# Performance work log

Measured on AMD Instinct MI355X. Metric: run time of the kernel, lower is better.

The kernel has to match this reference:

```python
import jax, jax.numpy as jnp
import numpy as np

B, N, H = 4, 1024, 64

def setup_inputs() -> dict:
    key = jax.random.key(0)
    k1, k2, k3 = jax.random.split(key, 3)
    x = jax.random.normal(k1, (B, N, H), dtype=jnp.float32)
    # nn.Linear(2H, H): weight [H, 2H], bias [H]
    s1 = 1.0 / np.sqrt(2 * H)
    W1 = jax.random.uniform(k2, (H, 2 * H), minval=-s1, maxval=s1, dtype=jnp.float32)
    b1 = jnp.zeros((H,), dtype=jnp.float32)
    # nn.Linear(H, 1): weight [1, H], bias [1]
    s2 = 1.0 / np.sqrt(H)
    W2 = jax.random.uniform(k3, (1, H), minval=-s2, maxval=s2, dtype=jnp.float32)
    b2 = jnp.zeros((1,), dtype=jnp.float32)
    return {"x": x, "W1": W1, "b1": b1, "W2": W2, "b2": b2}

def reference(x, W1, b1, W2, b2):
    # cat([x_i, x_j]) @ W1.T == x_i @ W1a.T + x_j @ W1b.T  (decomposed; same math)
    W1a, W1b = W1[:, :x.shape[-1]], W1[:, x.shape[-1]:]
    hi = jnp.einsum('bid,hd->bih', x, W1a)            # [B,N,H]
    hj = jnp.einsum('bjd,hd->bjh', x, W1b)            # [B,N,H]
    h = jax.nn.relu(hi[:, :, None, :] + hj[:, None, :, :] + b1)  # [B,N,N,H]
    logits = jnp.einsum('bijh,h->bij', h, W2[0]) + b2[0]          # [B,N,N]
    attn = jax.nn.softmax(logits, axis=-1)
    updated = jnp.einsum('bij,bjd->bid', attn, x)     # [B,N,H]
    return updated, attn
```

## Files before the change

kernel.cpp:

```cpp
#include <hip/hip_runtime.h>

#define ATTN_OFF 262144

#define WS_HIT   0
#define WS_HJT   262144
#define WS_LOG   524288
#define WS_SMAX  4718592
#define WS_SSUM  4784128
#define WS_ROWM  4849664
#define WS_ROWI  4853760
#define WS_PART  4857856

typedef float4 f4;
__device__ __forceinline__ f4 ld4(const float* p) { return *reinterpret_cast<const f4*>(p); }
__device__ __forceinline__ void st4(float* p, f4 v) { *reinterpret_cast<f4*>(p) = v; }

__global__ __launch_bounds__(256, 4)
void ka_proj(const float* __restrict__ x, const float* __restrict__ W1,
             const float* __restrict__ b1,
             float* __restrict__ hiT, float* __restrict__ hjT) {
    __shared__ float xT[64 * 68];
    __shared__ float w1T[64 * 68];
    const int t  = threadIdx.x;
    const int i0 = blockIdx.x * 64;
    const int b  = blockIdx.y;
    const int z  = blockIdx.z;
    const int lo = t & 15;
    const int dq = t >> 4;
#pragma unroll
    for (int p = 0; p < 4; ++p) {
        const int il = p * 16 + lo;
        f4 v = ld4(&x[(size_t)(b * 1024 + i0 + il) * 64 + dq * 4]);
        xT[(dq * 4 + 0) * 68 + il] = v.x;
        xT[(dq * 4 + 1) * 68 + il] = v.y;
        xT[(dq * 4 + 2) * 68 + il] = v.z;
        xT[(dq * 4 + 3) * 68 + il] = v.w;
        f4 w = ld4(&W1[(size_t)il * 128 + z * 64 + dq * 4]);
        w1T[(dq * 4 + 0) * 68 + il] = w.x;
        w1T[(dq * 4 + 1) * 68 + il] = w.y;
        w1T[(dq * 4 + 2) * 68 + il] = w.z;
        w1T[(dq * 4 + 3) * 68 + il] = w.w;
    }
    __syncthreads();
    const int tx = t & 15;
    const int ty = t >> 4;
    float acc[4][4];
    if (z == 0) {
        f4 bv = ld4(&b1[tx * 4]);
        float ba[4] = {bv.x, bv.y, bv.z, bv.w};
#pragma unroll
        for (int ii = 0; ii < 4; ++ii)
#pragma unroll
            for (int cc = 0; cc < 4; ++cc) acc[ii][cc] = ba[cc];
    } else {
#pragma unroll
        for (int ii = 0; ii < 4; ++ii)
#pragma unroll
            for (int cc = 0; cc < 4; ++cc) acc[ii][cc] = 0.f;
    }
#pragma unroll 8
    for (int d = 0; d < 64; ++d) {
        f4 xv = ld4(&xT[d * 68 + ty * 4]);
        f4 wv = ld4(&w1T[d * 68 + tx * 4]);
        float xa[4] = {xv.x, xv.y, xv.z, xv.w};
        float wa[4] = {wv.x, wv.y, wv.z, wv.w};
#pragma unroll
        for (int ii = 0; ii < 4; ++ii)
#pragma unroll
            for (int cc = 0; cc < 4; ++cc)
                acc[ii][cc] = fmaf(xa[ii], wa[cc], acc[ii][cc]);
    }
    float* outp = z ? hjT : hiT;
#pragma unroll
    for (int cc = 0; cc < 4; ++cc) {
        f4 o = make_float4(acc[0][cc], acc[1][cc], acc[2][cc], acc[3][cc]);
        st4(&outp[(size_t)(b * 64 + tx * 4 + cc) * 1024 + i0 + ty * 4], o);
    }
}

__global__ __launch_bounds__(256, 2)
void kb_logits(const float* __restrict__ hiT, const float* __restrict__ hjT,
               const float* __restrict__ W2, float* __restrict__ logits,
               float* __restrict__ smax, float* __restrict__ ssum) {
    __shared__ float s_hi[64 * 128];
    __shared__ float s_hj[64 * 64];
    __shared__ float s_w2[64];
    const int t  = threadIdx.x;
    const int jT = blockIdx.x;
    const int iT = blockIdx.y;
    const int b  = blockIdx.z;
#pragma unroll
    for (int p = 0; p < 8; ++p) {
        const int idx = p * 256 + t;
        const int h   = idx >> 5;
        const int c4  = (idx & 31) * 4;
        st4(&s_hi[h * 128 + c4], ld4(&hiT[(size_t)(b * 64 + h) * 1024 + iT * 128 + c4]));
    }
#pragma unroll
    for (int p = 0; p < 4; ++p) {
        const int idx = p * 256 + t;
        const int h   = idx >> 4;
        const int c4  = (idx & 15) * 4;
        st4(&s_hj[h * 64 + c4], ld4(&hjT[(size_t)(b * 64 + h) * 1024 + jT * 64 + c4]));
    }
    if (t < 16) st4(&s_w2[t * 4], ld4(&W2[t * 4]));
    __syncthreads();
    const int tx = t & 15;
    const int ty = t >> 4;
    float acc[8][4];
#pragma unroll
    for (int ii = 0; ii < 8; ++ii)
#pragma unroll
        for (int jj = 0; jj < 4; ++jj) acc[ii][jj] = 0.f;
#pragma unroll 2
    for (int h = 0; h < 64; ++h) {
        f4 a0 = ld4(&s_hi[h * 128 + ty * 8]);
        f4 a1 = ld4(&s_hi[h * 128 + ty * 8 + 4]);
        f4 bv = ld4(&s_hj[h * 64 + tx * 4]);
        const float w = s_w2[h];
        float aa[8] = {a0.x, a0.y, a0.z, a0.w, a1.x, a1.y, a1.z, a1.w};
        float bb[4] = {bv.x, bv.y, bv.z, bv.w};
#pragma unroll
        for (int ii = 0; ii < 8; ++ii)
#pragma unroll
            for (int jj = 0; jj < 4; ++jj)
                acc[ii][jj] = fmaf(fmaxf(aa[ii] + bb[jj], 0.f), w, acc[ii][jj]);
    }
#pragma unroll
    for (int ii = 0; ii < 8; ++ii) {
        const int row = b * 1024 + iT * 128 + ty * 8 + ii;
        f4 o = make_float4(acc[ii][0], acc[ii][1], acc[ii][2], acc[ii][3]);
        st4(&logits[(size_t)row * 1024 + jT * 64 + tx * 4], o);
        float m = fmaxf(fmaxf(acc[ii][0], acc[ii][1]), fmaxf(acc[ii][2], acc[ii][3]));
#pragma unroll
        for (int d = 1; d < 16; d <<= 1) m = fmaxf(m, __shfl_xor(m, d));
        float s = __expf(acc[ii][0] - m) + __expf(acc[ii][1] - m) +
                  __expf(acc[ii][2] - m) + __expf(acc[ii][3] - m);
#pragma unroll
        for (int d = 1; d < 16; d <<= 1) s += __shfl_xor(s, d);
        if (tx == 0) {
            smax[jT * 4096 + row] = m;
            ssum[jT * 4096 + row] = s;
        }
    }
}

__global__ __launch_bounds__(256)
void kredux(const float* __restrict__ smax, const float* __restrict__ ssum,
            float* __restrict__ rowM, float* __restrict__ rowInv) {
    const int r = blockIdx.x * 256 + threadIdx.x;
    float mv[16], sv[16];
#pragma unroll
    for (int c = 0; c < 16; ++c) { mv[c] = smax[c * 4096 + r]; sv[c] = ssum[c * 4096 + r]; }
    float M = mv[0];
#pragma unroll
    for (int c = 1; c < 16; ++c) M = fmaxf(M, mv[c]);
    float L = 0.f;
#pragma unroll
    for (int c = 0; c < 16; ++c) L += sv[c] * __expf(mv[c] - M);
    rowM[r]   = M;
    rowInv[r] = 1.0f / L;
}

__global__ __launch_bounds__(256)
void kd_av(const float* __restrict__ logits, const float* __restrict__ rowM,
           const float* __restrict__ rowInv, const float* __restrict__ x,
           float* __restrict__ attn, float* __restrict__ part) {
    __shared__ float s_p[64 * 260];
    __shared__ float s_x[64 * 64];
    __shared__ float s_m[256];
    __shared__ float s_il[256];
    const int t  = threadIdx.x;
    const int ks = blockIdx.x;
    const int iT = blockIdx.y;
    const int b  = blockIdx.z;
    const int i0 = iT * 256;
    const int j0 = ks * 64;
    const int gr = b * 1024 + i0;
    s_m[t]  = rowM[gr + t];
    s_il[t] = rowInv[gr + t];
#pragma unroll
    for (int p = 0; p < 4; ++p) {
        const int idx = p * 256 + t;
        const int j   = idx >> 4;
        const int d4  = (idx & 15) * 4;
        st4(&s_x[j * 64 + d4], ld4(&x[(size_t)(b * 1024 + j0 + j) * 64 + d4]));
    }
    __syncthreads();
#pragma unroll 4
    for (int it = 0; it < 16; ++it) {
        const int idx = it * 256 + t;
        const int rl  = idx >> 4;
        const int j4  = (idx & 15) * 4;
        f4 v = ld4(&logits[(size_t)(gr + rl) * 1024 + j0 + j4]);
        const float m  = s_m[rl];
        const float il = s_il[rl];
        f4 pv;
        pv.x = __expf(v.x - m) * il;
        pv.y = __expf(v.y - m) * il;
        pv.z = __expf(v.z - m) * il;
        pv.w = __expf(v.w - m) * il;
        st4(&attn[(size_t)(gr + rl) * 1024 + j0 + j4], pv);
        s_p[(j4 + 0) * 260 + rl] = pv.x;
        s_p[(j4 + 1) * 260 + rl] = pv.y;
        s_p[(j4 + 2) * 260 + rl] = pv.z;
        s_p[(j4 + 3) * 260 + rl] = pv.w;
    }
    __syncthreads();
    const int tx = t & 7;
    const int ty = t >> 3;
    float acc[8][8];
#pragma unroll
    for (int ii = 0; ii < 8; ++ii)
#pragma unroll
        for (int dd = 0; dd < 8; ++dd) acc[ii][dd] = 0.f;
#pragma unroll 2
    for (int j = 0; j < 64; ++j) {
        f4 a0 = ld4(&s_p[j * 260 + ty * 8]);
        f4 a1 = ld4(&s_p[j * 260 + ty * 8 + 4]);
        f4 b0 = ld4(&s_x[j * 64 + tx * 8]);
        f4 b1 = ld4(&s_x[j * 64 + tx * 8 + 4]);
        float aa[8] = {a0.x, a0.y, a0.z, a0.w, a1.x, a1.y, a1.z, a1.w};
        float bb[8] = {b0.x, b0.y, b0.z, b0.w, b1.x, b1.y, b1.z, b1.w};
#pragma unroll
        for (int ii = 0; ii < 8; ++ii)
#pragma unroll
            for (int dd = 0; dd < 8; ++dd)
                acc[ii][dd] = fmaf(aa[ii], bb[dd], acc[ii][dd]);
    }
#pragma unroll
    for (int ii = 0; ii < 8; ++ii) {
        const size_t o = (size_t)(ks * 4096 + gr + ty * 8 + ii) * 64 + tx * 8;
        st4(&part[o],     make_float4(acc[ii][0], acc[ii][1], acc[ii][2], acc[ii][3]));
        st4(&part[o + 4], make_float4(acc[ii][4], acc[ii][5], acc[ii][6], acc[ii][7]));
    }
}

__global__ __launch_bounds__(256)
void ke_reduce(const float* __restrict__ part, float* __restrict__ out) {
    const int g = blockIdx.x * 256 + threadIdx.x;
    f4 a = ld4(&part[(size_t)g * 4]);
#pragma unroll
    for (int ks = 1; ks < 16; ++ks) {
        f4 v = ld4(&part[(size_t)ks * 262144 + g * 4]);
        a.x += v.x; a.y += v.y; a.z += v.z; a.w += v.w;
    }
    st4(&out[(size_t)g * 4], a);
}

extern "C" void kernel_launch(void* const* d_in, const int* in_sizes, int n_in,
                              void* d_out, int out_size, void* d_ws, size_t ws_size,
                              hipStream_t stream) {
    const float* x  = (const float*)d_in[0];
    const float* W1 = (const float*)d_in[1];
    const float* b1 = (const float*)d_in[2];
    const float* W2 = (const float*)d_in[3];
    float* out = (float*)d_out;
    float* ws  = (float*)d_ws;
    float* hiT    = ws + WS_HIT;
    float* hjT    = ws + WS_HJT;
    float* logits = ws + WS_LOG;
    float* smax   = ws + WS_SMAX;
    float* ssum   = ws + WS_SSUM;
    float* rowM   = ws + WS_ROWM;
    float* rowInv = ws + WS_ROWI;
    float* part   = ws + WS_PART;

    ka_proj  <<<dim3(16, 4, 2),  256, 0, stream>>>(x, W1, b1, hiT, hjT);
    kb_logits<<<dim3(16, 8, 4),  256, 0, stream>>>(hiT, hjT, W2, logits, smax, ssum);
    kredux   <<<dim3(16),        256, 0, stream>>>(smax, ssum, rowM, rowInv);
    kd_av    <<<dim3(16, 4, 4),  256, 0, stream>>>(logits, rowM, rowInv, x,
                                                   out + ATTN_OFF, part);
    ke_reduce<<<dim3(256),       256, 0, stream>>>(part, out);
}
```

Measured before the change: 118.3 us.

## Switch pairwise logits and AV to packed fp16 dot2, fuse reductions with atomics

Stores the projections, logits and the probability/x tiles as packed fp16 and uses v_dot2 (fp16 pairs accumulated in fp32) for both the relu-weighted logit sum and the attn@x product. This halves the logits workspace traffic and shared-memory footprint. It folds the row max/sum reduction into kd_av and replaces the split-K partial buffer and its reduce kernel with atomicAdd into an output zeroed by ka_proj, cutting two launches. The cost is reduced precision in the logits and attention weights, and nondeterministic float atomics.

```diff
diff --git a/kernel.cpp b/kernel.cpp
--- a/kernel.cpp
+++ b/kernel.cpp
@@ -2,29 +2,44 @@
 
 #define ATTN_OFF 262144
 
-#define WS_HIT   0
-#define WS_HJT   262144
-#define WS_LOG   524288
-#define WS_SMAX  4718592
-#define WS_SSUM  4784128
-#define WS_ROWM  4849664
-#define WS_ROWI  4853760
-#define WS_PART  4857856
+#define WS_HIP  0
+#define WS_HJP  131072
+#define WS_L16  262144
+#define WS_SMAX 2359296
+#define WS_SSUM 2424832
 
 typedef float4 f4;
+typedef _Float16 h2v __attribute__((ext_vector_type(2)));
+
+union F4H { f4 f; h2v h[4]; };
+union F2H { float2 f; h2v h[2]; };
+
 __device__ __forceinline__ f4 ld4(const float* p) { return *reinterpret_cast<const f4*>(p); }
 __device__ __forceinline__ void st4(float* p, f4 v) { *reinterpret_cast<f4*>(p) = v; }
+__device__ __forceinline__ float fdot2f(h2v a, h2v b, float c) {
+    return __builtin_amdgcn_fdot2(a, b, c, false);
+}
+__device__ __forceinline__ h2v pack2(float a, float b) {
+    h2v r; r.x = (_Float16)a; r.y = (_Float16)b; return r;
+}
 
 __global__ __launch_bounds__(256, 4)
 void ka_proj(const float* __restrict__ x, const float* __restrict__ W1,
              const float* __restrict__ b1,
-             float* __restrict__ hiT, float* __restrict__ hjT) {
+             h2v* __restrict__ hiP, h2v* __restrict__ hjP, float* __restrict__ outz) {
     __shared__ float xT[64 * 68];
     __shared__ float w1T[64 * 68];
     const int t  = threadIdx.x;
     const int i0 = blockIdx.x * 64;
     const int b  = blockIdx.y;
     const int z  = blockIdx.z;
+    {
+        const int bid = blockIdx.x + blockIdx.y * 16 + blockIdx.z * 64;
+        const int zi  = (bid * 256 + t) * 2;
+        f4 zv = make_float4(0.f, 0.f, 0.f, 0.f);
+        st4(&outz[(size_t)zi * 4], zv);
+        st4(&outz[(size_t)(zi + 1) * 4], zv);
+    }
     const int lo = t & 15;
     const int dq = t >> 4;
 #pragma unroll
@@ -70,40 +85,49 @@
             for (int cc = 0; cc < 4; ++cc)
                 acc[ii][cc] = fmaf(xa[ii], wa[cc], acc[ii][cc]);
     }
-    float* outp = z ? hjT : hiT;
-#pragma unroll
-    for (int cc = 0; cc < 4; ++cc) {
-        f4 o = make_float4(acc[0][cc], acc[1][cc], acc[2][cc], acc[3][cc]);
-        st4(&outp[(size_t)(b * 64 + tx * 4 + cc) * 1024 + i0 + ty * 4], o);
-    }
-}
-
-__global__ __launch_bounds__(256, 2)
-void kb_logits(const float* __restrict__ hiT, const float* __restrict__ hjT,
-               const float* __restrict__ W2, float* __restrict__ logits,
+    h2v* outp = z ? hjP : hiP;
+#pragma unroll
+    for (int p = 0; p < 2; ++p) {
+        F4H u;
+#pragma unroll
+        for (int ii = 0; ii < 4; ++ii)
+            u.h[ii] = pack2(acc[ii][p * 2 + 0], acc[ii][p * 2 + 1]);
+        st4((float*)&outp[(size_t)(b * 32 + tx * 2 + p) * 1024 + i0 + ty * 4], u.f);
+    }
+}
+
+__global__ __launch_bounds__(256, 4)
+void kb_logits(const h2v* __restrict__ hiP, const h2v* __restrict__ hjP,
+               const float* __restrict__ W2, _Float16* __restrict__ l16,
                float* __restrict__ smax, float* __restrict__ ssum) {
-    __shared__ float s_hi[64 * 128];
-    __shared__ float s_hj[64 * 64];
-    __shared__ float s_w2[64];
+    __shared__ __align__(16) h2v s_hi[32 * 128];
+    __shared__ __align__(16) h2v s_hj[32 * 64];
+    __shared__ h2v s_w2[32];
     const int t  = threadIdx.x;
     const int jT = blockIdx.x;
     const int iT = blockIdx.y;
     const int b  = blockIdx.z;
 #pragma unroll
-    for (int p = 0; p < 8; ++p) {
-        const int idx = p * 256 + t;
-        const int h   = idx >> 5;
-        const int c4  = (idx & 31) * 4;
-        st4(&s_hi[h * 128 + c4], ld4(&hiT[(size_t)(b * 64 + h) * 1024 + iT * 128 + c4]));
-    }
-#pragma unroll
     for (int p = 0; p < 4; ++p) {
         const int idx = p * 256 + t;
-        const int h   = idx >> 4;
+        const int hp  = idx >> 5;
+        const int c4  = (idx & 31) * 4;
+        st4((float*)&s_hi[hp * 128 + c4],
+            ld4((const float*)&hiP[(size_t)(b * 32 + hp) * 1024 + iT * 128 + c4]));
+    }
+#pragma unroll
+    for (int p = 0; p < 2; ++p) {
+        const int idx = p * 256 + t;
+        const int hp  = idx >> 4;
         const int c4  = (idx & 15) * 4;
-        st4(&s_hj[h * 64 + c4], ld4(&hjT[(size_t)(b * 64 + h) * 1024 + jT * 64 + c4]));
-    }
-    if (t < 16) st4(&s_w2[t * 4], ld4(&W2[t * 4]));
+        st4((float*)&s_hj[hp * 64 + c4],
+            ld4((const float*)&hjP[(size_t)(b * 32 + hp) * 1024 + jT * 64 + c4]));
+    }
+    if (t < 16) {
+        f4 w = ld4(&W2[t * 4]);
+        s_w2[t * 2]     = pack2(w.x, w.y);
+        s_w2[t * 2 + 1] = pack2(w.z, w.w);
+    }
     __syncthreads();
     const int tx = t & 15;
     const int ty = t >> 4;
@@ -112,25 +136,31 @@
     for (int ii = 0; ii < 8; ++ii)
 #pragma unroll
         for (int jj = 0; jj < 4; ++jj) acc[ii][jj] = 0.f;
-#pragma unroll 2
-    for (int h = 0; h < 64; ++h) {
-        f4 a0 = ld4(&s_hi[h * 128 + ty * 8]);
-        f4 a1 = ld4(&s_hi[h * 128 + ty * 8 + 4]);
-        f4 bv = ld4(&s_hj[h * 64 + tx * 4]);
-        const float w = s_w2[h];
-        float aa[8] = {a0.x, a0.y, a0.z, a0.w, a1.x, a1.y, a1.z, a1.w};
-        float bb[4] = {bv.x, bv.y, bv.z, bv.w};
-#pragma unroll
-        for (int ii = 0; ii < 8; ++ii)
-#pragma unroll
-            for (int jj = 0; jj < 4; ++jj)
-                acc[ii][jj] = fmaf(fmaxf(aa[ii] + bb[jj], 0.f), w, acc[ii][jj]);
+    const h2v z2 = (h2v)0;
+#pragma unroll 4
+    for (int hp = 0; hp < 32; ++hp) {
+        F4H a0, a1, bb;
+        a0.f = ld4((const float*)&s_hi[hp * 128 + ty * 8]);
+        a1.f = ld4((const float*)&s_hi[hp * 128 + ty * 8 + 4]);
+        bb.f = ld4((const float*)&s_hj[hp * 64 + tx * 4]);
+        const h2v w2p = s_w2[hp];
+#pragma unroll
+        for (int ii = 0; ii < 8; ++ii) {
+            const h2v av = (ii < 4) ? a0.h[ii] : a1.h[ii - 4];
+#pragma unroll
+            for (int jj = 0; jj < 4; ++jj) {
+                h2v r = __builtin_elementwise_max(av + bb.h[jj], z2);
+                acc[ii][jj] = fdot2f(r, w2p, acc[ii][jj]);
+            }
+        }
     }
 #pragma unroll
     for (int ii = 0; ii < 8; ++ii) {
         const int row = b * 1024 + iT * 128 + ty * 8 + ii;
-        f4 o = make_float4(acc[ii][0], acc[ii][1], acc[ii][2], acc[ii][3]);
-        st4(&logits[(size_t)row * 1024 + jT * 64 + tx * 4], o);
+        F2H uo;
+        uo.h[0] = pack2(acc[ii][0], acc[ii][1]);
+        uo.h[1] = pack2(acc[ii][2], acc[ii][3]);
+        *reinterpret_cast<float2*>(&l16[(size_t)row * 1024 + jT * 64 + tx * 4]) = uo.f;
         float m = fmaxf(fmaxf(acc[ii][0], acc[ii][1]), fmaxf(acc[ii][2], acc[ii][3]));
 #pragma unroll
         for (int d = 1; d < 16; d <<= 1) m = fmaxf(m, __shfl_xor(m, d));
@@ -145,66 +175,72 @@
     }
 }
 
+#define PSTR 260
 __global__ __launch_bounds__(256)
-void kredux(const float* __restrict__ smax, const float* __restrict__ ssum,
-            float* __restrict__ rowM, float* __restrict__ rowInv) {
-    const int r = blockIdx.x * 256 + threadIdx.x;
-    float mv[16], sv[16];
-#pragma unroll
-    for (int c = 0; c < 16; ++c) { mv[c] = smax[c * 4096 + r]; sv[c] = ssum[c * 4096 + r]; }
-    float M = mv[0];
-#pragma unroll
-    for (int c = 1; c < 16; ++c) M = fmaxf(M, mv[c]);
-    float L = 0.f;
-#pragma unroll
-    for (int c = 0; c < 16; ++c) L += sv[c] * __expf(mv[c] - M);
-    rowM[r]   = M;
-    rowInv[r] = 1.0f / L;
-}
-
-__global__ __launch_bounds__(256)
-void kd_av(const float* __restrict__ logits, const float* __restrict__ rowM,
-           const float* __restrict__ rowInv, const float* __restrict__ x,
-           float* __restrict__ attn, float* __restrict__ part) {
-    __shared__ float s_p[64 * 260];
-    __shared__ float s_x[64 * 64];
+void kd_av(const _Float16* __restrict__ l16, const float* __restrict__ smax,
+           const float* __restrict__ ssum, const float* __restrict__ x,
+           float* __restrict__ attn, float* __restrict__ out) {
+    __shared__ __align__(16) h2v s_p[32 * PSTR];
+    __shared__ __align__(16) h2v s_x[32 * 64];
     __shared__ float s_m[256];
     __shared__ float s_il[256];
     const int t  = threadIdx.x;
     const int ks = blockIdx.x;
     const int iT = blockIdx.y;
     const int b  = blockIdx.z;
-    const int i0 = iT * 256;
     const int j0 = ks * 64;
-    const int gr = b * 1024 + i0;
-    s_m[t]  = rowM[gr + t];
-    s_il[t] = rowInv[gr + t];
-#pragma unroll
-    for (int p = 0; p < 4; ++p) {
-        const int idx = p * 256 + t;
-        const int j   = idx >> 4;
+    const int gr = b * 1024 + iT * 256;
+    {
+        float mv[16], sv[16];
+#pragma unroll
+        for (int c = 0; c < 16; ++c) {
+            mv[c] = smax[c * 4096 + gr + t];
+            sv[c] = ssum[c * 4096 + gr + t];
+        }
+        float M = mv[0];
+#pragma unroll
+        for (int c = 1; c < 16; ++c) M = fmaxf(M, mv[c]);
+        float L = 0.f;
+#pragma unroll
+        for (int c = 0; c < 16; ++c) L += sv[c] * __expf(mv[c] - M);
+        s_m[t]  = M;
+        s_il[t] = 1.0f / L;
+    }
+#pragma unroll
+    for (int it = 0; it < 2; ++it) {
+        const int idx = it * 256 + t;
+        const int jp  = idx >> 4;
         const int d4  = (idx & 15) * 4;
-        st4(&s_x[j * 64 + d4], ld4(&x[(size_t)(b * 1024 + j0 + j) * 64 + d4]));
-    }
-    __syncthreads();
-#pragma unroll 4
-    for (int it = 0; it < 16; ++it) {
+        f4 r0 = ld4(&x[(size_t)(b * 1024 + j0 + jp * 2)     * 64 + d4]);
+        f4 r1 = ld4(&x[(size_t)(b * 1024 + j0 + jp * 2 + 1) * 64 + d4]);
+        F4H u;
+        u.h[0] = pack2(r0.x, r1.x); u.h[1] = pack2(r0.y, r1.y);
+        u.h[2] = pack2(r0.z, r1.z); u.h[3] = pack2(r0.w, r1.w);
+        st4((float*)&s_x[jp * 64 + d4], u.f);
+    }
+    __syncthreads();
+#pragma unroll 2
+    for (int it = 0; it < 8; ++it) {
         const int idx = it * 256 + t;
-        const int rl  = idx >> 4;
-        const int j4  = (idx & 15) * 4;
-        f4 v = ld4(&logits[(size_t)(gr + rl) * 1024 + j0 + j4]);
+        const int rl  = idx >> 3;
+        const int j8  = (idx & 7) * 8;
+        F4H u;
+        u.f = ld4((const float*)&l16[(size_t)(gr + rl) * 1024 + j0 + j8]);
         const float m  = s_m[rl];
         const float il = s_il[rl];
-        f4 pv;
-        pv.x = __expf(v.x - m) * il;
-        pv.y = __expf(v.y - m) * il;
-        pv.z = __expf(v.z - m) * il;
-        pv.w = __expf(v.w - m) * il;
-        st4(&attn[(size_t)(gr + rl) * 1024 + j0 + j4], pv);
-        s_p[(j4 + 0) * 260 + rl] = pv.x;
-        s_p[(j4 + 1) * 260 + rl] = pv.y;
-        s_p[(j4 + 2) * 260 + rl] = pv.z;
-        s_p[(j4 + 3) * 260 + rl] = pv.w;
+        float p[8];
+#pragma unroll
+        for (int k = 0; k < 4; ++k) {
+            p[2 * k]     = __expf((float)u.h[k].x - m) * il;
+            p[2 * k + 1] = __expf((float)u.h[k].y - m) * il;
+        }
+        float* ap = &attn[(size_t)(gr + rl) * 1024 + j0 + j8];
+        st4(ap,     make_float4(p[0], p[1], p[2], p[3]));
+        st4(ap + 4, make_float4(p[4], p[5], p[6], p[7]));
+        const int jp0 = (idx & 7) * 4;
+#pragma unroll
+        for (int k = 0; k < 4; ++k)
+            s_p[(jp0 + k) * PSTR + rl] = pack2(p[2 * k], p[2 * k + 1]);
     }
     __syncthreads();
     const int tx = t & 7;
@@ -214,38 +250,26 @@
     for (int ii = 0; ii < 8; ++ii)
 #pragma unroll
         for (int dd = 0; dd < 8; ++dd) acc[ii][dd] = 0.f;
-#pragma unroll 2
-    for (int j = 0; j < 64; ++j) {
-        f4 a0 = ld4(&s_p[j * 260 + ty * 8]);
-        f4 a1 = ld4(&s_p[j * 260 + ty * 8 + 4]);
-        f4 b0 = ld4(&s_x[j * 64 + tx * 8]);
-        f4 b1 = ld4(&s_x[j * 64 + tx * 8 + 4]);
-        float aa[8] = {a0.x, a0.y, a0.z, a0.w, a1.x, a1.y, a1.z, a1.w};
-        float bb[8] = {b0.x, b0.y, b0.z, b0.w, b1.x, b1.y, b1.z, b1.w};
+#pragma unroll 4
+    for (int jp = 0; jp < 32; ++jp) {
+        F4H a0, a1, x0, x1;
+        a0.f = ld4((const float*)&s_p[jp * PSTR + ty * 8]);
+        a1.f = ld4((const float*)&s_p[jp * PSTR + ty * 8 + 4]);
+        x0.f = ld4((const float*)&s_x[jp * 64 + tx * 8]);
+        x1.f = ld4((const float*)&s_x[jp * 64 + tx * 8 + 4]);
+        h2v aa[8] = {a0.h[0], a0.h[1], a0.h[2], a0.h[3], a1.h[0], a1.h[1], a1.h[2], a1.h[3]};
+        h2v xx[8] = {x0.h[0], x0.h[1], x0.h[2], x0.h[3], x1.h[0], x1.h[1], x1.h[2], x1.h[3]};
 #pragma unroll
         for (int ii = 0; ii < 8; ++ii)
 #pragma unroll
             for (int dd = 0; dd < 8; ++dd)
-                acc[ii][dd] = fmaf(aa[ii], bb[dd], acc[ii][dd]);
-    }
-#pragma unroll
-    for (int ii = 0; ii < 8; ++ii) {
-        const size_t o = (size_t)(ks * 4096 + gr + ty * 8 + ii) * 64 + tx * 8;
-        st4(&part[o],     make_float4(acc[ii][0], acc[ii][1], acc[ii][2], acc[ii][3]));
-        st4(&part[o + 4], make_float4(acc[ii][4], acc[ii][5], acc[ii][6], acc[ii][7]));
-    }
-}
-
-__global__ __launch_bounds__(256)
-void ke_reduce(const float* __restrict__ part, float* __restrict__ out) {
-    const int g = blockIdx.x * 256 + threadIdx.x;
-    f4 a = ld4(&part[(size_t)g * 4]);
-#pragma unroll
-    for (int ks = 1; ks < 16; ++ks) {
-        f4 v = ld4(&part[(size_t)ks * 262144 + g * 4]);
-        a.x += v.x; a.y += v.y; a.z += v.z; a.w += v.w;
-    }
-    st4(&out[(size_t)g * 4], a);
+                acc[ii][dd] = fdot2f(aa[ii], xx[dd], acc[ii][dd]);
+    }
+#pragma unroll
+    for (int ii = 0; ii < 8; ++ii)
+#pragma unroll
+        for (int dd = 0; dd < 8; ++dd)
+            atomicAdd(&out[(size_t)(gr + ty * 8 + ii) * 64 + tx * 8 + dd], acc[ii][dd]);
 }
 
 extern "C" void kernel_launch(void* const* d_in, const int* in_sizes, int n_in,
@@ -257,19 +281,14 @@
     const float* W2 = (const float*)d_in[3];
     float* out = (float*)d_out;
     float* ws  = (float*)d_ws;
-    float* hiT    = ws + WS_HIT;
-    float* hjT    = ws + WS_HJT;
-    float* logits = ws + WS_LOG;
-    float* smax   = ws + WS_SMAX;
-    float* ssum   = ws + WS_SSUM;
-    float* rowM   = ws + WS_ROWM;
-    float* rowInv = ws + WS_ROWI;
-    float* part   = ws + WS_PART;
-
-    ka_proj  <<<dim3(16, 4, 2),  256, 0, stream>>>(x, W1, b1, hiT, hjT);
-    kb_logits<<<dim3(16, 8, 4),  256, 0, stream>>>(hiT, hjT, W2, logits, smax, ssum);
-    kredux   <<<dim3(16),        256, 0, stream>>>(smax, ssum, rowM, rowInv);
-    kd_av    <<<dim3(16, 4, 4),  256, 0, stream>>>(logits, rowM, rowInv, x,
-                                                   out + ATTN_OFF, part);
-    ke_reduce<<<dim3(256),       256, 0, stream>>>(part, out);
-}
+    h2v*      hiP  = (h2v*)(ws + WS_HIP);
+    h2v*      hjP  = (h2v*)(ws + WS_HJP);
+    _Float16* l16  = (_Float16*)(ws + WS_L16);
+    float*    smax = ws + WS_SMAX;
+    float*    ssum = ws + WS_SSUM;
+
+    ka_proj  <<<dim3(16, 4, 2), 256, 0, stream>>>(x, W1, b1, hiP, hjP, out);
+    kb_logits<<<dim3(16, 8, 4), 256, 0, stream>>>(hiP, hjP, W2, l16, smax, ssum);
+    kd_av    <<<dim3(16, 4, 4), 256, 0, stream>>>(l16, smax, ssum, x,
+                                                  out + ATTN_OFF, out);
+}
```

Measured after the change: 215.2 us. +82.0%, slower.
